# Kernel optimization log

Measured on AMD Instinct MI355X. Metric: run time of the kernel, lower is better.

Reference implementation:

```python
import jax, jax.numpy as jnp
import numpy as np
from jax import lax

D_MODEL = 1024
D_STATE = 16
D_CONV = 4
D_INNER = 2 * D_MODEL
B_SZ = 2
L_SEQ = 1024
EPS = 1e-5


def setup_inputs() -> dict:
    key = jax.random.key(0)
    ks = jax.random.split(key, 8)
    s = lambda k, shape, scale: jax.random.normal(k, shape, jnp.float32) * scale
    return {
        "x": jax.random.normal(ks[0], (B_SZ, L_SEQ, D_MODEL), jnp.float32),
        "norm_w": jnp.ones((D_MODEL,), jnp.float32),
        "norm_b": jnp.zeros((D_MODEL,), jnp.float32),
        "in_proj_w": s(ks[1], (2 * D_INNER, D_MODEL), 0.02),
        "in_proj_b": jnp.zeros((2 * D_INNER,), jnp.float32),
        "conv_w": s(ks[2], (D_INNER, 1, D_CONV), 0.1),   # torch Conv1d weight (out, in/groups, k)
        "conv_b": jnp.zeros((D_INNER,), jnp.float32),
        "x_proj_w": s(ks[3], (2 * D_STATE, D_INNER), 0.02),
        "x_proj_b": jnp.zeros((2 * D_STATE,), jnp.float32),
        "dt_proj_w": s(ks[4], (D_INNER, D_INNER), 0.02),
        "dt_proj_b": jnp.zeros((D_INNER,), jnp.float32),
        "A_log": s(ks[5], (D_INNER, D_STATE), 1.0),
        "D_param": jnp.ones((D_INNER,), jnp.float32),
        "out_proj_w": s(ks[6], (D_MODEL, D_INNER), 0.02),
        "out_proj_b": jnp.zeros((D_MODEL,), jnp.float32),
    }


def _layernorm(x, w, b):
    mu = jnp.mean(x, axis=-1, keepdims=True)
    var = jnp.mean(jnp.square(x - mu), axis=-1, keepdims=True)
    return (x - mu) * lax.rsqrt(var + EPS) * w + b


def _silu(x):
    return x * jax.nn.sigmoid(x)


def _selective_scan(u, delta, A, B_ssm, C_ssm):
    # u, delta: (B, L, d_inner); A: (d_inner, d_state); B_ssm, C_ssm: (B, L, d_state)
    dA = jnp.exp(delta[..., None] * A)                    # (B, L, d_inner, d_state)
    dBu = (delta * u)[..., None] * B_ssm[:, :, None, :]   # (B, L, d_inner, d_state)
    # time-major for scan
    dA_t = jnp.moveaxis(dA, 1, 0)
    dBu_t = jnp.moveaxis(dBu, 1, 0)
    C_t = jnp.moveaxis(C_ssm, 1, 0)

    def step(h, inp):
        dA_i, dBu_i, c_i = inp
        h = dA_i * h + dBu_i                              # (B, d_inner, d_state)
        y = jnp.einsum('bds,bs->bd', h, c_i)
        return h, y

    h0 = jnp.zeros((u.shape[0], u.shape[2], A.shape[1]), u.dtype)
    _, ys = lax.scan(step, h0, (dA_t, dBu_t, C_t))
    return jnp.moveaxis(ys, 0, 1)                         # (B, L, d_inner)


def reference(x, norm_w, norm_b, in_proj_w, in_proj_b, conv_w, conv_b,
              x_proj_w, x_proj_b, dt_proj_w, dt_proj_b, A_log, D_param,
              out_proj_w, out_proj_b):
    residual = x
    xn = _layernorm(x, norm_w, norm_b)
    xz = xn @ in_proj_w.T + in_proj_b                     # (B, L, 2*d_inner)
    xc, z = jnp.split(xz, 2, axis=-1)
    # depthwise causal conv1d (torch pads both sides d_conv-1 then slices :L == left pad)
    kern = jnp.transpose(conv_w, (2, 1, 0))               # (k, 1, d_inner) for 'LIO'
    xc = lax.conv_general_dilated(
        xc, kern, window_strides=(1,), padding=[(D_CONV - 1, 0)],
        dimension_numbers=('NLC', 'LIO', 'NLC'), feature_group_count=D_INNER) + conv_b
    u = _silu(xc)
    x_db = u @ x_proj_w.T + x_proj_b                      # (B, L, 2*d_state)
    B_ssm, C_ssm = jnp.split(x_db, 2, axis=-1)
    delta = jax.nn.softplus(u @ dt_proj_w.T + dt_proj_b)  # (B, L, d_inner)
    A = -jnp.exp(A_log)
    y = _selective_scan(u, delta, A, B_ssm, C_ssm)
    y = y + u * D_param
    y = y * _silu(z)
    out = y @ out_proj_w.T + out_proj_b
    return residual + out
```

## Files before the change

### kernel.cpp

```cpp
#include <hip/hip_runtime.h>

#define DM   1024
#define DI   2048
#define LSEQ 1024
#define BSZ  2
#define MROWS (BSZ*LSEQ)
#define NCH   (BSZ*DI)
#define SCHUNK 32
#define STEPS  32
#define PLANE  (NCH*16)

typedef __attribute__((ext_vector_type(4)))  float  f32x4;
typedef __attribute__((ext_vector_type(8)))  __bf16 bf16x8;

__device__ __forceinline__ unsigned short f2bf(float f) {
  union { float f; unsigned int u; } v; v.f = f;
  unsigned int u = v.u;
  unsigned int r = (u + 0x7fffu + ((u >> 16) & 1u)) >> 16;
  return (unsigned short)r;
}
__device__ __forceinline__ float bf2f(unsigned short h) {
  union { unsigned int u; float f; } v; v.u = (unsigned int)h << 16; return v.f;
}

__device__ __forceinline__ void load_lds16(const void* g, void* l) {
  __builtin_amdgcn_global_load_lds((const __attribute__((address_space(1))) void*)g,
                                   (__attribute__((address_space(3))) void*)l, 16, 0, 0);
}

__global__ __launch_bounds__(256) void ln_cast(const float* __restrict__ x,
    const float* __restrict__ w, const float* __restrict__ b,
    unsigned short* __restrict__ out)
{
  int row = blockIdx.x, tid = threadIdx.x;
  const float4* xr = (const float4*)(x + (size_t)row * DM);
  float4 v = xr[tid];
  float s  = v.x + v.y + v.z + v.w;
  float s2 = v.x*v.x + v.y*v.y + v.z*v.z + v.w*v.w;
  #pragma unroll
  for (int off = 32; off > 0; off >>= 1) { s += __shfl_down(s, off); s2 += __shfl_down(s2, off); }
  __shared__ float ss[4], sq[4];
  if ((tid & 63) == 0) { ss[tid >> 6] = s; sq[tid >> 6] = s2; }
  __syncthreads();
  float mean = (ss[0]+ss[1]+ss[2]+ss[3]) * (1.0f/DM);
  float var  = (sq[0]+sq[1]+sq[2]+sq[3]) * (1.0f/DM) - mean*mean;
  float rs = rsqrtf(var + 1e-5f);
  float4 wv = ((const float4*)w)[tid];
  float4 bv = ((const float4*)b)[tid];
  ushort4 o;
  o.x = f2bf((v.x-mean)*rs*wv.x + bv.x);
  o.y = f2bf((v.y-mean)*rs*wv.y + bv.y);
  o.z = f2bf((v.z-mean)*rs*wv.z + bv.z);
  o.w = f2bf((v.w-mean)*rs*wv.w + bv.w);
  ((ushort4*)(out + (size_t)row * DM))[tid] = o;
}

__global__ __launch_bounds__(256) void cast_all(
    const float* __restrict__ s0, unsigned short* __restrict__ d0,
    const float* __restrict__ s1, unsigned short* __restrict__ d1,
    const float* __restrict__ s2, unsigned short* __restrict__ d2,
    const float* __restrict__ s3, unsigned short* __restrict__ d3)
{
  const int N0 = 4096*1024/4, N1 = 2048*2048/4, N2 = 1024*2048/4, N3 = 32*2048/4;
  int i = blockIdx.x * 256 + threadIdx.x;
  int stride = gridDim.x * 256;
  int total = N0 + N1 + N2 + N3;
  for (; i < total; i += stride) {
    const float* s; unsigned short* d; int j = i;
    if (j < N0) { s = s0; d = d0; }
    else if ((j -= N0) < N1) { s = s1; d = d1; }
    else if ((j -= N1) < N2) { s = s2; d = d2; }
    else { j -= N2; s = s3; d = d3; }
    float4 v = ((const float4*)s)[j];
    ushort4 o;
    o.x = f2bf(v.x); o.y = f2bf(v.y); o.z = f2bf(v.z); o.w = f2bf(v.w);
    ((ushort4*)d)[j] = o;
  }
}

template<int EPI, typename OT>
__global__ __launch_bounds__(256) void gemm_bt(
    const unsigned short* __restrict__ A, const unsigned short* __restrict__ Bw,
    const float* __restrict__ bias, const float* __restrict__ resid,
    OT* __restrict__ C, int N, int K)
{
  __shared__ unsigned short As[2][128*64];
  __shared__ unsigned short Bs[2][64*64];
  const int tid  = threadIdx.x;
  const int lane = tid & 63;
  const int w    = tid >> 6;

  const int nbx = gridDim.x;
  const int nwg = gridDim.x * gridDim.y;
  int wg  = blockIdx.y * nbx + blockIdx.x;
  int swz = (wg & 7) * (nwg >> 3) + (wg >> 3);
  const int m0 = (swz / nbx) * 128;
  const int n0 = (swz % nbx) * 64;

  const int wm = w >> 1, wn = w & 1;
  const int r16 = lane & 15;
  const int kg  = lane >> 4;

  const int srow = tid >> 3;
  const int kl   = (tid & 7) ^ (srow & 7);
  const unsigned short* gaBase = A  + (size_t)(m0 + srow) * K + kl * 8;
  const unsigned short* gbBase = Bw + (size_t)(n0 + srow) * K + kl * 8;

  f32x4 acc[4][2] = {};

  auto stage = [&](int buf, int kt) {
    const unsigned short* ga = gaBase + kt;
    load_lds16(ga,                   (char*)As[buf] + tid*16);
    load_lds16(ga + (size_t)32*K,    (char*)As[buf] +  4096 + tid*16);
    load_lds16(ga + (size_t)64*K,    (char*)As[buf] +  8192 + tid*16);
    load_lds16(ga + (size_t)96*K,    (char*)As[buf] + 12288 + tid*16);
    const unsigned short* gb = gbBase + kt;
    load_lds16(gb,                   (char*)Bs[buf] + tid*16);
    load_lds16(gb + (size_t)32*K,    (char*)Bs[buf] +  4096 + tid*16);
  };

  stage(0, 0);
  stage(1, 64);

  int cur = 0;
  for (int kt = 0; kt < K; kt += 64) {
    if (kt + 64 < K) asm volatile("s_waitcnt vmcnt(6)" ::: "memory");
    else             asm volatile("s_waitcnt vmcnt(0)" ::: "memory");
    __builtin_amdgcn_s_barrier();

    bf16x8 av[2][4], bv[2][2];
    #pragma unroll
    for (int kk = 0; kk < 2; ++kk) {
      const int phys = (kk*4 + kg) ^ (r16 & 7);
      #pragma unroll
      for (int i = 0; i < 4; ++i)
        av[kk][i] = *(const bf16x8*)((const char*)As[cur] + (wm*64 + i*16 + r16)*128 + phys*16);
      #pragma unroll
      for (int j = 0; j < 2; ++j)
        bv[kk][j] = *(const bf16x8*)((const char*)Bs[cur] + (wn*32 + j*16 + r16)*128 + phys*16);
    }
    #pragma unroll
    for (int kk = 0; kk < 2; ++kk)
      #pragma unroll
      for (int i = 0; i < 4; ++i)
        #pragma unroll
        for (int j = 0; j < 2; ++j)
          acc[i][j] = __builtin_amdgcn_mfma_f32_16x16x32_bf16(av[kk][i], bv[kk][j], acc[i][j], 0, 0, 0);

    asm volatile("s_waitcnt lgkmcnt(0)" ::: "memory");
    __builtin_amdgcn_s_barrier();
    if (kt + 128 < K) stage(cur, kt + 128);
    cur ^= 1;
  }

  #pragma unroll
  for (int i = 0; i < 4; ++i) {
    int rbase = m0 + wm*64 + i*16 + kg*4;
    #pragma unroll
    for (int j = 0; j < 2; ++j) {
      int col = n0 + wn*32 + j*16 + r16;
      float bcol = bias[col];
      #pragma unroll
      for (int r = 0; r < 4; ++r) {
        int row = rbase + r;
        float v = acc[i][j][r] + bcol;
        if (EPI == 1) v = (v > 20.f) ? v : log1pf(__expf(v));
        if (EPI == 2) v += resid[(size_t)row * N + col];
        if constexpr (sizeof(OT) == 2) C[(size_t)row * N + col] = f2bf(v);
        else                           C[(size_t)row * N + col] = v;
      }
    }
  }
}

__global__ __launch_bounds__(256) void conv_silu(const unsigned short* __restrict__ xz,
    const float* __restrict__ cw, const float* __restrict__ cb,
    unsigned short* __restrict__ u_bf)
{
  int idx = blockIdx.x * 256 + threadIdx.x;
  int d = idx & (DI-1);
  int m = idx >> 11;
  int l = m & (LSEQ-1);
  const unsigned short* col = xz + (size_t)m * (2*DI) + d;
  float acc = cb[d];
  float w0 = cw[d*4+0], w1 = cw[d*4+1], w2 = cw[d*4+2], w3 = cw[d*4+3];
  acc += w3 * bf2f(col[0]);
  if (l >= 1) acc += w2 * bf2f(col[-(2*DI)]);
  if (l >= 2) acc += w1 * bf2f(col[-2*(2*DI)]);
  if (l >= 3) acc += w0 * bf2f(col[-3*(2*DI)]);
  float s = acc / (1.f + __expf(-acc));
  u_bf[idx] = f2bf(s);
}

__global__ __launch_bounds__(64) void xproj_mfma(const unsigned short* __restrict__ u_bf,
    const unsigned short* __restrict__ wx, const float* __restrict__ bias,
    float* __restrict__ xdb)
{
  int lane = threadIdx.x;
  int m0 = blockIdx.x * 16;
  int r16 = lane & 15, kg = lane >> 4;
  f32x4 acc0 = {}, acc1 = {};
  const unsigned short* ap  = u_bf + (size_t)(m0 + r16) * DI + kg*8;
  const unsigned short* b0p = wx   + (size_t)r16        * DI + kg*8;
  const unsigned short* b1p = wx   + (size_t)(16 + r16) * DI + kg*8;
  #pragma unroll 4
  for (int kt = 0; kt < DI; kt += 32) {
    bf16x8 a  = *(const bf16x8*)(ap  + kt);
    bf16x8 b0 = *(const bf16x8*)(b0p + kt);
    bf16x8 b1 = *(const bf16x8*)(b1p + kt);
    acc0 = __builtin_amdgcn_mfma_f32_16x16x32_bf16(a, b0, acc0, 0, 0, 0);
    acc1 = __builtin_amdgcn_mfma_f32_16x16x32_bf16(a, b1, acc1, 0, 0, 0);
  }
  #pragma unroll
  for (int r = 0; r < 4; ++r) {
    int row = m0 + kg*4 + r;
    xdb[row*32 + r16]      = acc0[r] + bias[r16];
    xdb[row*32 + 16 + r16] = acc1[r] + bias[16 + r16];
  }
}

__global__ __launch_bounds__(256) void scan_p1(const unsigned short* __restrict__ delta,
    const unsigned short* __restrict__ u, const float* __restrict__ xdb,
    const float* __restrict__ A_log, float* __restrict__ agg_a, float* __restrict__ agg_b)
{
  int tid = threadIdx.x;
  int sh  = tid & 3;
  int ch  = blockIdx.x * 64 + (tid >> 2);
  int c   = blockIdx.y;
  int b = ch >> 11, d = ch & (DI-1);
  float Ads[4];
  {
    f32x4 Ar = *(const f32x4*)(A_log + d*16 + sh*4);
    #pragma unroll
    for (int s = 0; s < 4; ++s) Ads[s] = -__expf(Ar[s]);
  }
  float a[4] = {1.f,1.f,1.f,1.f}, bb[4] = {0.f,0.f,0.f,0.f};
  int row0 = b * LSEQ + c * STEPS;
  const unsigned short* dp = delta + (size_t)row0 * DI + d;
  const unsigned short* up = u     + (size_t)row0 * DI + d;
  #pragma unroll 4
  for (int t = 0; t < STEPS; ++t) {
    float dl = bf2f(dp[t*DI]);
    float uu = bf2f(up[t*DI]);
    f32x4 Bv = *(const f32x4*)(xdb + (size_t)(row0 + t) * 32 + sh*4);
    float dlu = dl * uu;
    #pragma unroll
    for (int s = 0; s < 4; ++s) {
      float dA = __expf(dl * Ads[s]);
      bb[s] = fmaf(dA, bb[s], dlu * Bv[s]);
      a[s] *= dA;
    }
  }
  int idx = c*PLANE + ch*16 + sh*4;
  f32x4 av, bv;
  #pragma unroll
  for (int s = 0; s < 4; ++s) { av[s] = a[s]; bv[s] = bb[s]; }
  *(f32x4*)(agg_a + idx) = av;
  *(f32x4*)(agg_b + idx) = bv;
}

__global__ __launch_bounds__(256) void scan_p2(const float* __restrict__ agg_a,
    const float* __restrict__ agg_b, float* __restrict__ hinit)
{
  int idx = blockIdx.x * 256 + threadIdx.x;
  float h = 0.f;
  #pragma unroll
  for (int c = 0; c < SCHUNK; ++c) {
    hinit[c*PLANE + idx] = h;
    h = fmaf(agg_a[c*PLANE + idx], h, agg_b[c*PLANE + idx]);
  }
}

__global__ __launch_bounds__(256) void scan_p3(const unsigned short* __restrict__ delta,
    const unsigned short* __restrict__ u, const float* __restrict__ xdb,
    const float* __restrict__ A_log, const float* __restrict__ Dp,
    const unsigned short* __restrict__ xz, const float* __restrict__ hinit,
    unsigned short* __restrict__ y_bf)
{
  int tid = threadIdx.x;
  int sh  = tid & 3;
  int ch  = blockIdx.x * 64 + (tid >> 2);
  int c   = blockIdx.y;
  int b = ch >> 11, d = ch & (DI-1);
  float Ads[4];
  {
    f32x4 Ar = *(const f32x4*)(A_log + d*16 + sh*4);
    #pragma unroll
    for (int s = 0; s < 4; ++s) Ads[s] = -__expf(Ar[s]);
  }
  float h[4];
  {
    f32x4 hv = *(const f32x4*)(hinit + c*PLANE + ch*16 + sh*4);
    #pragma unroll
    for (int s = 0; s < 4; ++s) h[s] = hv[s];
  }
  float Dd = Dp[d];
  int row0 = b * LSEQ + c * STEPS;
  const unsigned short* dp = delta + (size_t)row0 * DI + d;
  const unsigned short* up = u     + (size_t)row0 * DI + d;
  const unsigned short* zp = xz    + (size_t)row0 * (2*DI) + DI + d;
  unsigned short* yp = y_bf + (size_t)row0 * DI + d;
  #pragma unroll 2
  for (int t = 0; t < STEPS; ++t) {
    float dl = bf2f(dp[t*DI]);
    float uu = bf2f(up[t*DI]);
    const float* xr = xdb + (size_t)(row0 + t) * 32 + sh*4;
    f32x4 Bv = *(const f32x4*)xr;
    f32x4 Cv = *(const f32x4*)(xr + 16);
    float dlu = dl * uu;
    float y = 0.f;
    #pragma unroll
    for (int s = 0; s < 4; ++s) {
      float dA = __expf(dl * Ads[s]);
      h[s] = fmaf(dA, h[s], dlu * Bv[s]);
      y = fmaf(h[s], Cv[s], y);
    }
    y += __shfl_xor(y, 1);
    y += __shfl_xor(y, 2);
    if (sh == 0) {
      float zz = bf2f(zp[t*(2*DI)]);
      float yv = y + uu * Dd;
      yv *= zz / (1.f + __expf(-zz));
      yp[t*DI] = f2bf(yv);
    }
  }
}

extern "C" void kernel_launch(void* const* d_in, const int* in_sizes, int n_in,
                              void* d_out, int out_size, void* d_ws, size_t ws_size,
                              hipStream_t stream)
{
  (void)in_sizes; (void)n_in; (void)out_size;
  const float* x      = (const float*)d_in[0];
  const float* norm_w = (const float*)d_in[1];
  const float* norm_b = (const float*)d_in[2];
  const float* in_w   = (const float*)d_in[3];
  const float* in_b   = (const float*)d_in[4];
  const float* conv_w = (const float*)d_in[5];
  const float* conv_b = (const float*)d_in[6];
  const float* xp_w   = (const float*)d_in[7];
  const float* xp_b   = (const float*)d_in[8];
  const float* dt_w   = (const float*)d_in[9];
  const float* dt_b   = (const float*)d_in[10];
  const float* A_log  = (const float*)d_in[11];
  const float* D_par  = (const float*)d_in[12];
  const float* out_w  = (const float*)d_in[13];
  const float* out_b  = (const float*)d_in[14];
  float* out = (float*)d_out;

  char* p = (char*)d_ws;
  unsigned short* xn_bf = (unsigned short*)p;  p += 2048ull*1024*2;
  unsigned short* w_in  = (unsigned short*)p;  p += 4096ull*1024*2;
  unsigned short* w_dt  = (unsigned short*)p;  p += 2048ull*2048*2;
  unsigned short* w_out = (unsigned short*)p;  p += 1024ull*2048*2;
  unsigned short* wx_bf = (unsigned short*)p;  p += 32ull*2048*2;
  unsigned short* xz    = (unsigned short*)p;  p += 2048ull*4096*2;
  unsigned short* u_bf  = (unsigned short*)p;  p += 2048ull*2048*2;
  float*          xdb   = (float*)p;           p += 2048ull*32*4;
  unsigned short* delta = (unsigned short*)p;  p += 2048ull*2048*2;
  unsigned short* y_bf  = (unsigned short*)p;  p += 2048ull*2048*2;
  float*          hinit = (float*)p;           p += (size_t)PLANE*SCHUNK*4;
  if ((size_t)(p - (char*)d_ws) > ws_size) return;

  float* agg_a = (float*)w_in;
  float* agg_b = (float*)w_dt;

  cast_all<<<2048, 256, 0, stream>>>(in_w, w_in, dt_w, w_dt, out_w, w_out, xp_w, wx_bf);
  ln_cast<<<MROWS, 256, 0, stream>>>(x, norm_w, norm_b, xn_bf);

  gemm_bt<0, unsigned short><<<dim3(4096/64, MROWS/128), 256, 0, stream>>>(xn_bf, w_in, in_b, nullptr, xz, 4096, 1024);
  conv_silu<<<(MROWS*DI)/256, 256, 0, stream>>>(xz, conv_w, conv_b, u_bf);
  xproj_mfma<<<MROWS/16, 64, 0, stream>>>(u_bf, wx_bf, xp_b, xdb);
  gemm_bt<1, unsigned short><<<dim3(2048/64, MROWS/128), 256, 0, stream>>>(u_bf, w_dt, dt_b, nullptr, delta, 2048, 2048);

  scan_p1<<<dim3(NCH/64, SCHUNK), 256, 0, stream>>>(delta, u_bf, xdb, A_log, agg_a, agg_b);
  scan_p2<<<PLANE/256, 256, 0, stream>>>(agg_a, agg_b, hinit);
  scan_p3<<<dim3(NCH/64, SCHUNK), 256, 0, stream>>>(delta, u_bf, xdb, A_log, D_par, xz, hinit, y_bf);

  gemm_bt<2, float><<<dim3(1024/64, MROWS/128), 256, 0, stream>>>(y_bf, w_out, out_b, x, out, 1024, 2048);
}
```

Before: 211.5 us.

## Fuse fp32-to-bf16 weight cast into GEMM B-tile staging

Removes the separate pass that cast the large in_proj, dt_proj and out_proj weights to bf16. Each GEMM now loads fp32 weight tiles into registers, converts them to bf16 and writes them to LDS, with a two-stage register prefetch. This drops a full read-and-write pass over about 14M weight elements, but doubles the global bytes read for the B operand and adds conversion ALU work inside the GEMM loop. The scan scratch buffers get their own workspace instead of aliasing the freed weight buffers.

Result: slower. 221.6 us (+4.8%).

```diff
diff --git a/kernel.cpp b/kernel.cpp
--- a/kernel.cpp
+++ b/kernel.cpp
@@ -55,32 +55,22 @@
   ((ushort4*)(out + (size_t)row * DM))[tid] = o;
 }
 
-__global__ __launch_bounds__(256) void cast_all(
-    const float* __restrict__ s0, unsigned short* __restrict__ d0,
-    const float* __restrict__ s1, unsigned short* __restrict__ d1,
-    const float* __restrict__ s2, unsigned short* __restrict__ d2,
-    const float* __restrict__ s3, unsigned short* __restrict__ d3)
-{
-  const int N0 = 4096*1024/4, N1 = 2048*2048/4, N2 = 1024*2048/4, N3 = 32*2048/4;
+__global__ __launch_bounds__(256) void castk(const float* __restrict__ in,
+    unsigned short* __restrict__ out, int n4)
+{
   int i = blockIdx.x * 256 + threadIdx.x;
   int stride = gridDim.x * 256;
-  int total = N0 + N1 + N2 + N3;
-  for (; i < total; i += stride) {
-    const float* s; unsigned short* d; int j = i;
-    if (j < N0) { s = s0; d = d0; }
-    else if ((j -= N0) < N1) { s = s1; d = d1; }
-    else if ((j -= N1) < N2) { s = s2; d = d2; }
-    else { j -= N2; s = s3; d = d3; }
-    float4 v = ((const float4*)s)[j];
+  for (; i < n4; i += stride) {
+    float4 v = ((const float4*)in)[i];
     ushort4 o;
     o.x = f2bf(v.x); o.y = f2bf(v.y); o.z = f2bf(v.z); o.w = f2bf(v.w);
-    ((ushort4*)d)[j] = o;
+    ((ushort4*)out)[i] = o;
   }
 }
 
 template<int EPI, typename OT>
 __global__ __launch_bounds__(256) void gemm_bt(
-    const unsigned short* __restrict__ A, const unsigned short* __restrict__ Bw,
+    const unsigned short* __restrict__ A, const float* __restrict__ Bw,
     const float* __restrict__ bias, const float* __restrict__ resid,
     OT* __restrict__ C, int N, int K)
 {
@@ -104,53 +94,72 @@
   const int srow = tid >> 3;
   const int kl   = (tid & 7) ^ (srow & 7);
   const unsigned short* gaBase = A  + (size_t)(m0 + srow) * K + kl * 8;
-  const unsigned short* gbBase = Bw + (size_t)(n0 + srow) * K + kl * 8;
+  const float*          gbBase = Bw + (size_t)(n0 + srow) * K + kl * 8;
 
   f32x4 acc[4][2] = {};
-
-  auto stage = [&](int buf, int kt) {
-    const unsigned short* ga = gaBase + kt;
-    load_lds16(ga,                   (char*)As[buf] + tid*16);
-    load_lds16(ga + (size_t)32*K,    (char*)As[buf] +  4096 + tid*16);
-    load_lds16(ga + (size_t)64*K,    (char*)As[buf] +  8192 + tid*16);
-    load_lds16(ga + (size_t)96*K,    (char*)As[buf] + 12288 + tid*16);
-    const unsigned short* gb = gbBase + kt;
-    load_lds16(gb,                   (char*)Bs[buf] + tid*16);
-    load_lds16(gb + (size_t)32*K,    (char*)Bs[buf] +  4096 + tid*16);
-  };
-
-  stage(0, 0);
-  stage(1, 64);
-
-  int cur = 0;
-  for (int kt = 0; kt < K; kt += 64) {
-    if (kt + 64 < K) asm volatile("s_waitcnt vmcnt(6)" ::: "memory");
-    else             asm volatile("s_waitcnt vmcnt(0)" ::: "memory");
-    __builtin_amdgcn_s_barrier();
-
-    bf16x8 av[2][4], bv[2][2];
-    #pragma unroll
-    for (int kk = 0; kk < 2; ++kk) {
-      const int phys = (kk*4 + kg) ^ (r16 & 7);
-      #pragma unroll
-      for (int i = 0; i < 4; ++i)
-        av[kk][i] = *(const bf16x8*)((const char*)As[cur] + (wm*64 + i*16 + r16)*128 + phys*16);
-      #pragma unroll
-      for (int j = 0; j < 2; ++j)
-        bv[kk][j] = *(const bf16x8*)((const char*)Bs[cur] + (wn*32 + j*16 + r16)*128 + phys*16);
-    }
-    #pragma unroll
-    for (int kk = 0; kk < 2; ++kk)
-      #pragma unroll
-      for (int i = 0; i < 4; ++i)
-        #pragma unroll
-        for (int j = 0; j < 2; ++j)
-          acc[i][j] = __builtin_amdgcn_mfma_f32_16x16x32_bf16(av[kk][i], bv[kk][j], acc[i][j], 0, 0, 0);
-
-    asm volatile("s_waitcnt lgkmcnt(0)" ::: "memory");
-    __builtin_amdgcn_s_barrier();
-    if (kt + 128 < K) stage(cur, kt + 128);
-    cur ^= 1;
+  float4 bR0[4], bR1[4];
+
+#define STAGE_A(BUF, KT) {                                              \
+    const unsigned short* ga = gaBase + (KT);                           \
+    load_lds16(ga,                (char*)As[BUF] + tid*16);             \
+    load_lds16(ga + (size_t)32*K, (char*)As[BUF] +  4096 + tid*16);     \
+    load_lds16(ga + (size_t)64*K, (char*)As[BUF] +  8192 + tid*16);     \
+    load_lds16(ga + (size_t)96*K, (char*)As[BUF] + 12288 + tid*16); }
+
+#define LOAD_B(P, KT) {                                                 \
+    const float* gb = gbBase + (KT);                                    \
+    bR##P[0] = *(const float4*)(gb);                                    \
+    bR##P[1] = *(const float4*)(gb + 4);                                \
+    bR##P[2] = *(const float4*)(gb + (size_t)32*K);                     \
+    bR##P[3] = *(const float4*)(gb + (size_t)32*K + 4); }
+
+#define WRITE_B(BUF, P) {                                               \
+    bf16x8 v0, v1;                                                      \
+    v0[0]=(__bf16)bR##P[0].x; v0[1]=(__bf16)bR##P[0].y;                 \
+    v0[2]=(__bf16)bR##P[0].z; v0[3]=(__bf16)bR##P[0].w;                 \
+    v0[4]=(__bf16)bR##P[1].x; v0[5]=(__bf16)bR##P[1].y;                 \
+    v0[6]=(__bf16)bR##P[1].z; v0[7]=(__bf16)bR##P[1].w;                 \
+    v1[0]=(__bf16)bR##P[2].x; v1[1]=(__bf16)bR##P[2].y;                 \
+    v1[2]=(__bf16)bR##P[2].z; v1[3]=(__bf16)bR##P[2].w;                 \
+    v1[4]=(__bf16)bR##P[3].x; v1[5]=(__bf16)bR##P[3].y;                 \
+    v1[6]=(__bf16)bR##P[3].z; v1[7]=(__bf16)bR##P[3].w;                 \
+    *(bf16x8*)((char*)Bs[BUF] + tid*16)        = v0;                    \
+    *(bf16x8*)((char*)Bs[BUF] + 4096 + tid*16) = v1; }
+
+#define GSTEP(BUF, P, KT) {                                                  \
+    if ((KT) + 128 < K) asm volatile("s_waitcnt vmcnt(8)" ::: "memory");     \
+    else                asm volatile("s_waitcnt vmcnt(0)" ::: "memory");     \
+    WRITE_B(BUF, P);                                                         \
+    asm volatile("s_waitcnt lgkmcnt(0)" ::: "memory");                       \
+    __builtin_amdgcn_s_barrier();                                            \
+    bf16x8 av[2][4], bv[2][2];                                               \
+    _Pragma("unroll")                                                        \
+    for (int kk = 0; kk < 2; ++kk) {                                         \
+      const int phys = (kk*4 + kg) ^ (r16 & 7);                              \
+      _Pragma("unroll")                                                      \
+      for (int i = 0; i < 4; ++i)                                            \
+        av[kk][i] = *(const bf16x8*)((const char*)As[BUF] + (wm*64 + i*16 + r16)*128 + phys*16); \
+      _Pragma("unroll")                                                      \
+      for (int j = 0; j < 2; ++j)                                            \
+        bv[kk][j] = *(const bf16x8*)((const char*)Bs[BUF] + (wn*32 + j*16 + r16)*128 + phys*16); \
+    }                                                                        \
+    _Pragma("unroll")                                                        \
+    for (int kk = 0; kk < 2; ++kk)                                           \
+      _Pragma("unroll")                                                      \
+      for (int i = 0; i < 4; ++i)                                            \
+        _Pragma("unroll")                                                    \
+        for (int j = 0; j < 2; ++j)                                          \
+          acc[i][j] = __builtin_amdgcn_mfma_f32_16x16x32_bf16(av[kk][i], bv[kk][j], acc[i][j], 0, 0, 0); \
+    asm volatile("s_waitcnt lgkmcnt(0)" ::: "memory");                       \
+    __builtin_amdgcn_s_barrier();                                            \
+    if ((KT) + 128 < K) { STAGE_A(BUF, (KT) + 128); LOAD_B(P, (KT) + 128); } }
+
+  STAGE_A(0, 0);  LOAD_B(0, 0);
+  STAGE_A(1, 64); LOAD_B(1, 64);
+
+  for (int kt = 0; kt < K; kt += 128) {
+    GSTEP(0, 0, kt);
+    GSTEP(1, 1, kt + 64);
   }
 
   #pragma unroll
@@ -171,6 +180,10 @@
       }
     }
   }
+#undef GSTEP
+#undef WRITE_B
+#undef LOAD_B
+#undef STAGE_A
 }
 
 __global__ __launch_bounds__(256) void conv_silu(const unsigned short* __restrict__ xz,
@@ -350,32 +363,28 @@
 
   char* p = (char*)d_ws;
   unsigned short* xn_bf = (unsigned short*)p;  p += 2048ull*1024*2;
-  unsigned short* w_in  = (unsigned short*)p;  p += 4096ull*1024*2;
-  unsigned short* w_dt  = (unsigned short*)p;  p += 2048ull*2048*2;
-  unsigned short* w_out = (unsigned short*)p;  p += 1024ull*2048*2;
   unsigned short* wx_bf = (unsigned short*)p;  p += 32ull*2048*2;
   unsigned short* xz    = (unsigned short*)p;  p += 2048ull*4096*2;
   unsigned short* u_bf  = (unsigned short*)p;  p += 2048ull*2048*2;
   float*          xdb   = (float*)p;           p += 2048ull*32*4;
   unsigned short* delta = (unsigned short*)p;  p += 2048ull*2048*2;
   unsigned short* y_bf  = (unsigned short*)p;  p += 2048ull*2048*2;
+  float*          agg_a = (float*)p;           p += (size_t)PLANE*SCHUNK*4;
+  float*          agg_b = (float*)p;           p += (size_t)PLANE*SCHUNK*4;
   float*          hinit = (float*)p;           p += (size_t)PLANE*SCHUNK*4;
   if ((size_t)(p - (char*)d_ws) > ws_size) return;
 
-  float* agg_a = (float*)w_in;
-  float* agg_b = (float*)w_dt;
-
-  cast_all<<<2048, 256, 0, stream>>>(in_w, w_in, dt_w, w_dt, out_w, w_out, xp_w, wx_bf);
+  castk<<<64, 256, 0, stream>>>(xp_w, wx_bf, 32*2048/4);
   ln_cast<<<MROWS, 256, 0, stream>>>(x, norm_w, norm_b, xn_bf);
 
-  gemm_bt<0, unsigned short><<<dim3(4096/64, MROWS/128), 256, 0, stream>>>(xn_bf, w_in, in_b, nullptr, xz, 4096, 1024);
+  gemm_bt<0, unsigned short><<<dim3(4096/64, MROWS/128), 256, 0, stream>>>(xn_bf, in_w, in_b, nullptr, xz, 4096, 1024);
   conv_silu<<<(MROWS*DI)/256, 256, 0, stream>>>(xz, conv_w, conv_b, u_bf);
   xproj_mfma<<<MROWS/16, 64, 0, stream>>>(u_bf, wx_bf, xp_b, xdb);
-  gemm_bt<1, unsigned short><<<dim3(2048/64, MROWS/128), 256, 0, stream>>>(u_bf, w_dt, dt_b, nullptr, delta, 2048, 2048);
+  gemm_bt<1, unsigned short><<<dim3(2048/64, MROWS/128), 256, 0, stream>>>(u_bf, dt_w, dt_b, nullptr, delta, 2048, 2048);
 
   scan_p1<<<dim3(NCH/64, SCHUNK), 256, 0, stream>>>(delta, u_bf, xdb, A_log, agg_a, agg_b);
   scan_p2<<<PLANE/256, 256, 0, stream>>>(agg_a, agg_b, hinit);
   scan_p3<<<dim3(NCH/64, SCHUNK), 256, 0, stream>>>(delta, u_bf, xdb, A_log, D_par, xz, hinit, y_bf);
 
-  gemm_bt<2, float><<<dim3(1024/64, MROWS/128), 256, 0, stream>>>(y_bf, w_out, out_b, x, out, 1024, 2048);
-}
+  gemm_bt<2, float><<<dim3(1024/64, MROWS/128), 256, 0, stream>>>(y_bf, out_w, out_b, x, out, 1024, 2048);
+}
```
